# Kernel optimization log

Hardware: AMD Instinct MI355X
Metric: run time of the kernel (lower is better)

## Reference

```python
import jax, jax.numpy as jnp
import numpy as np

H = 4096      # hidden_size (also vocab size of the embedding, per source)
O = 4096      # output_size (also embedding dim, per source)
MAX_LEN = 15


def setup_inputs() -> dict:
    key = jax.random.key(0)
    ks = jax.random.split(key, 16)
    s = 0.02  # init scale
    inp = {
        "input_ids": jax.random.randint(ks[0], (1,), 0, H),
        "hidden": jax.random.normal(ks[1], (1, 1, H), jnp.float32),
        "e_output": jax.random.normal(ks[2], (1, H), jnp.float32),   # unused, kept for signature fidelity
        "e_output_seq": jax.random.normal(ks[3], (MAX_LEN, H), jnp.float32),
        # parameters
        "emb_W": jax.random.normal(ks[4], (H, O), jnp.float32) * s,
        "att_W": jax.random.normal(ks[5], (MAX_LEN, H + O), jnp.float32) * s,
        "att_b": jnp.zeros((MAX_LEN,), jnp.float32),
        "comb_W": jax.random.normal(ks[6], (H, H + O), jnp.float32) * s,
        "comb_b": jnp.zeros((H,), jnp.float32),
        "gru_W_ih": jax.random.normal(ks[7], (3 * H, H), jnp.float32) * s,
        "gru_W_hh": jax.random.normal(ks[8], (3 * H, H), jnp.float32) * s,
        "gru_b_ih": jnp.zeros((3 * H,), jnp.float32),
        "gru_b_hh": jnp.zeros((3 * H,), jnp.float32),
        "out_W": jax.random.normal(ks[9], (O, H), jnp.float32) * s,
        "out_b": jnp.zeros((O,), jnp.float32),
    }
    return inp


def reference(input_ids, hidden, e_output, e_output_seq, emb_W, att_W, att_b,
              comb_W, comb_b, gru_W_ih, gru_W_hh, gru_b_ih, gru_b_hh, out_W, out_b):
    # dropout is identity in eval mode
    emb = emb_W[input_ids[0]][None, :]                       # [1, O]
    h0 = hidden[0]                                            # [1, H]
    att_logits = jnp.concatenate([emb, h0], axis=1) @ att_W.T + att_b
    att_weights = jax.nn.softmax(att_logits, axis=-1)         # [1, MAX_LEN]
    att_applied = att_weights @ e_output_seq                   # [1, H]
    combined = jnp.concatenate([emb, att_applied], axis=1)     # [1, H+O]
    x = jax.nn.relu(combined @ comb_W.T + comb_b)              # [1, H]
    # GRU cell (PyTorch gate order: r, z, n)
    gi = x @ gru_W_ih.T + gru_b_ih                             # [1, 3H]
    gh = h0 @ gru_W_hh.T + gru_b_hh                            # [1, 3H]
    i_r, i_z, i_n = jnp.split(gi, 3, axis=1)
    h_r, h_z, h_n = jnp.split(gh, 3, axis=1)
    r = jax.nn.sigmoid(i_r + h_r)
    z = jax.nn.sigmoid(i_z + h_z)
    n = jnp.tanh(i_n + r * h_n)
    h_new = (1.0 - z) * n + z * h0                             # [1, H]
    out = jax.nn.log_softmax(h_new @ out_W.T + out_b, axis=-1)  # [1, O]
    return out, h_new[None, :, :], att_weights
```

## Files before the change

### kernel.cpp

```cpp
#include <hip/hip_runtime.h>

#define H 4096
#define O 4096
#define HO 8192
#define MAXLEN 15

__device__ __forceinline__ void wave_dot2(const float* __restrict__ w0,
                                          const float* __restrict__ w1,
                                          const float* __restrict__ x,
                                          int n4, int lane,
                                          float& r0, float& r1) {
    const float4* a  = (const float4*)w0;
    const float4* b  = (const float4*)w1;
    const float4* xx = (const float4*)x;
    float acc0 = 0.f, acc1 = 0.f;
    #pragma unroll 4
    for (int i = lane; i < n4; i += 64) {
        float4 xv = xx[i];
        float4 av = a[i];
        float4 bv = b[i];
        acc0 += av.x * xv.x + av.y * xv.y + av.z * xv.z + av.w * xv.w;
        acc1 += bv.x * xv.x + bv.y * xv.y + bv.z * xv.z + bv.w * xv.w;
    }
    #pragma unroll
    for (int off = 32; off; off >>= 1) {
        acc0 += __shfl_down(acc0, off, 64);
        acc1 += __shfl_down(acc1, off, 64);
    }
    r0 = acc0; r1 = acc1;
}

__global__ __launch_bounds__(1024) void k_attlogit(const int* __restrict__ ids,
                                                   const float* __restrict__ hidden,
                                                   const float* __restrict__ embW,
                                                   const float* __restrict__ attW,
                                                   const float* __restrict__ attb,
                                                   float* __restrict__ attlog) {
    __shared__ float sred[16];
    const int tid = threadIdx.x, lane = tid & 63, wave = tid >> 6;
    const int j = blockIdx.x;
    const float* emb = embW + (size_t)ids[0] * O;
    const float4* w4 = (const float4*)(attW + (size_t)j * (H + O));
    const float4* e4 = (const float4*)emb;
    const float4* h4 = (const float4*)hidden;

    float4 wv0 = w4[tid];
    float4 xv0 = e4[tid];
    float4 wv1 = w4[tid + 1024];
    float4 xv1 = h4[tid];
    float acc = wv0.x * xv0.x + wv0.y * xv0.y + wv0.z * xv0.z + wv0.w * xv0.w
              + wv1.x * xv1.x + wv1.y * xv1.y + wv1.z * xv1.z + wv1.w * xv1.w;
    #pragma unroll
    for (int off = 32; off; off >>= 1) acc += __shfl_down(acc, off, 64);
    if (lane == 0) sred[wave] = acc;
    __syncthreads();
    if (tid == 0) {
        float s = 0.f;
        #pragma unroll
        for (int w = 0; w < 16; w++) s += sred[w];
        attlog[j] = s + attb[j];
    }
}

__global__ __launch_bounds__(256) void k_attapply(const int* __restrict__ ids,
                                                  const float* __restrict__ embW,
                                                  const float* __restrict__ attlog,
                                                  const float* __restrict__ eseq,
                                                  float* __restrict__ combined,
                                                  float* __restrict__ out_attw) {
    const int k = blockIdx.x * 256 + threadIdx.x;
    float l[MAXLEN];
    float m = -1e30f;
    #pragma unroll
    for (int j = 0; j < MAXLEN; j++) { l[j] = attlog[j]; m = fmaxf(m, l[j]); }
    float s = 0.f;
    #pragma unroll
    for (int j = 0; j < MAXLEN; j++) { l[j] = __expf(l[j] - m); s += l[j]; }
    const float inv = 1.f / s;

    float acc = 0.f;
    #pragma unroll
    for (int j = 0; j < MAXLEN; j++) acc += l[j] * eseq[j * H + k];
    combined[O + k] = acc * inv;
    combined[k] = embW[(size_t)ids[0] * O + k];
    if (blockIdx.x == 0 && threadIdx.x < MAXLEN) out_attw[threadIdx.x] = l[threadIdx.x] * inv;
}

__global__ __launch_bounds__(512) void k_mv1(const float* __restrict__ combW,
                                             const float* __restrict__ combB,
                                             const float* __restrict__ ghhW,
                                             const float* __restrict__ ghhB,
                                             const float* __restrict__ hidden,
                                             const float* __restrict__ combined,
                                             float* __restrict__ xout,
                                             float* __restrict__ ghout) {
    const int wave = threadIdx.x >> 6, lane = threadIdx.x & 63;
    const int b = blockIdx.x;
    float r0, r1;
    if (b < 256) {
        const int row = b * 16 + wave * 2;
        wave_dot2(combW + (size_t)row * HO, combW + (size_t)(row + 1) * HO,
                  combined, HO >> 2, lane, r0, r1);
        if (lane == 0) {
            xout[row]     = fmaxf(r0 + combB[row], 0.f);
            xout[row + 1] = fmaxf(r1 + combB[row + 1], 0.f);
        }
    } else {
        const int row = (b - 256) * 16 + wave * 2;
        wave_dot2(ghhW + (size_t)row * H, ghhW + (size_t)(row + 1) * H,
                  hidden, H >> 2, lane, r0, r1);
        if (lane == 0) {
            ghout[row]     = r0 + ghhB[row];
            ghout[row + 1] = r1 + ghhB[row + 1];
        }
    }
}

__global__ __launch_bounds__(256) void k_gru(const float* __restrict__ gihW,
                                             const float* __restrict__ gihB,
                                             const float* __restrict__ hidden,
                                             const float* __restrict__ x,
                                             const float* __restrict__ gh,
                                             float* __restrict__ hout,
                                             float* __restrict__ out_h) {
    const int wave = threadIdx.x >> 6, lane = threadIdx.x & 63;
    const int i = blockIdx.x * 4 + wave;
    const float4* w0 = (const float4*)(gihW + (size_t)i * H);
    const float4* w1 = (const float4*)(gihW + (size_t)(i + H) * H);
    const float4* w2 = (const float4*)(gihW + (size_t)(i + 2 * H) * H);
    const float4* x4 = (const float4*)x;
    float a0 = 0.f, a1 = 0.f, a2 = 0.f;
    #pragma unroll 4
    for (int t = lane; t < (H >> 2); t += 64) {
        float4 xv = x4[t];
        float4 v0 = w0[t];
        float4 v1 = w1[t];
        float4 v2 = w2[t];
        a0 += v0.x * xv.x + v0.y * xv.y + v0.z * xv.z + v0.w * xv.w;
        a1 += v1.x * xv.x + v1.y * xv.y + v1.z * xv.z + v1.w * xv.w;
        a2 += v2.x * xv.x + v2.y * xv.y + v2.z * xv.z + v2.w * xv.w;
    }
    #pragma unroll
    for (int off = 32; off; off >>= 1) {
        a0 += __shfl_down(a0, off, 64);
        a1 += __shfl_down(a1, off, 64);
        a2 += __shfl_down(a2, off, 64);
    }
    if (lane == 0) {
        float ir = a0 + gihB[i];
        float iz = a1 + gihB[i + H];
        float in_ = a2 + gihB[i + 2 * H];
        float hr = gh[i], hz = gh[i + H], hn = gh[i + 2 * H];
        float r = 1.f / (1.f + __expf(-(ir + hr)));
        float z = 1.f / (1.f + __expf(-(iz + hz)));
        float n = tanhf(in_ + r * hn);
        float h0 = hidden[i];
        float h = (1.f - z) * n + z * h0;
        hout[i] = h;
        out_h[i] = h;
    }
}

__global__ __launch_bounds__(512) void k_out(const float* __restrict__ outW,
                                             const float* __restrict__ outB,
                                             const float* __restrict__ h,
                                             float* __restrict__ logits) {
    const int wave = threadIdx.x >> 6, lane = threadIdx.x & 63;
    const int row = blockIdx.x * 16 + wave * 2;
    float r0, r1;
    wave_dot2(outW + (size_t)row * H, outW + (size_t)(row + 1) * H, h, H >> 2, lane, r0, r1);
    if (lane == 0) {
        logits[row]     = r0 + outB[row];
        logits[row + 1] = r1 + outB[row + 1];
    }
}

__global__ __launch_bounds__(1024) void k_lsm(const float* __restrict__ logits,
                                              float* __restrict__ out) {
    __shared__ float red[16];
    __shared__ float red2[16];
    const int tid = threadIdx.x, lane = tid & 63, wave = tid >> 6;
    float m = -1e30f;
    for (int k = tid; k < O; k += 1024) m = fmaxf(m, logits[k]);
    #pragma unroll
    for (int off = 32; off; off >>= 1) m = fmaxf(m, __shfl_down(m, off, 64));
    if (lane == 0) red[wave] = m;
    __syncthreads();
    if (tid == 0) {
        float mm = -1e30f;
        for (int j = 0; j < 16; j++) mm = fmaxf(mm, red[j]);
        red[0] = mm;
    }
    __syncthreads();
    m = red[0];
    float s = 0.f;
    for (int k = tid; k < O; k += 1024) s += __expf(logits[k] - m);
    #pragma unroll
    for (int off = 32; off; off >>= 1) s += __shfl_down(s, off, 64);
    if (lane == 0) red2[wave] = s;
    __syncthreads();
    if (tid == 0) {
        float ss = 0.f;
        for (int j = 0; j < 16; j++) ss += red2[j];
        red2[0] = m + logf(ss);
    }
    __syncthreads();
    float lse = red2[0];
    for (int k = tid; k < O; k += 1024) out[k] = logits[k] - lse;
}

extern "C" void kernel_launch(void* const* d_in, const int* in_sizes, int n_in,
                              void* d_out, int out_size, void* d_ws, size_t ws_size,
                              hipStream_t stream) {
    const int*   ids    = (const int*)d_in[0];
    const float* hidden = (const float*)d_in[1];
    const float* eseq   = (const float*)d_in[3];
    const float* embW   = (const float*)d_in[4];
    const float* attW   = (const float*)d_in[5];
    const float* attb   = (const float*)d_in[6];
    const float* combW  = (const float*)d_in[7];
    const float* combB  = (const float*)d_in[8];
    const float* gihW   = (const float*)d_in[9];
    const float* ghhW   = (const float*)d_in[10];
    const float* gihB   = (const float*)d_in[11];
    const float* ghhB   = (const float*)d_in[12];
    const float* outW   = (const float*)d_in[13];
    const float* outB   = (const float*)d_in[14];
    float* out = (float*)d_out;

    float* ws       = (float*)d_ws;
    float* combined = ws;
    float* xbuf     = ws + 8192;
    float* ghbuf    = ws + 12288;
    float* hbuf     = ws + 24576;
    float* logits   = ws + 28672;
    float* attlog   = ws + 32768;

    k_attlogit<<<MAXLEN, 1024, 0, stream>>>(ids, hidden, embW, attW, attb, attlog);
    k_attapply<<<16,     256,  0, stream>>>(ids, embW, attlog, eseq, combined, out + 8192);
    k_mv1     <<<1024,   512,  0, stream>>>(combW, combB, ghhW, ghhB, hidden, combined, xbuf, ghbuf);
    k_gru     <<<1024,   256,  0, stream>>>(gihW, gihB, hidden, xbuf, ghbuf, hbuf, out + 4096);
    k_out     <<<256,    512,  0, stream>>>(outW, outB, hbuf, logits);
    k_lsm     <<<1,      1024, 0, stream>>>(logits, out);
}
```

Measured before the change: 566.0 us.

## Stream GEMV weights through LDS with async double-buffered global_load_lds

```diff
diff --git a/kernel.cpp b/kernel.cpp
--- a/kernel.cpp
+++ b/kernel.cpp
@@ -4,30 +4,53 @@
 #define O 4096
 #define HO 8192
 #define MAXLEN 15
-
-__device__ __forceinline__ void wave_dot2(const float* __restrict__ w0,
-                                          const float* __restrict__ w1,
-                                          const float* __restrict__ x,
-                                          int n4, int lane,
-                                          float& r0, float& r1) {
-    const float4* a  = (const float4*)w0;
-    const float4* b  = (const float4*)w1;
-    const float4* xx = (const float4*)x;
+#define CHUNK 256
+
+typedef const __attribute__((address_space(1))) unsigned int* as1_u32p;
+typedef __attribute__((address_space(3))) unsigned int* as3_u32p;
+
+__device__ __forceinline__ void stage1k(const float* g, float* l) {
+    __builtin_amdgcn_global_load_lds((as1_u32p)g, (as3_u32p)l, 16, 0, 0);
+}
+
+#define WAITV(N) asm volatile("s_waitcnt vmcnt(" #N ")" ::: "memory")
+#define REGION_FENCE() do { asm volatile("" ::: "memory"); __builtin_amdgcn_sched_barrier(0); } while (0)
+
+__device__ __forceinline__ void mv2(const float* __restrict__ W, int row, int K, int NC,
+                                    const float* __restrict__ x, float* sst, int lane,
+                                    float& out0, float& out1) {
+    const float* wr0 = W + (size_t)row * K;
+    const float* wr1 = wr0 + K;
+    stage1k(wr0 + lane * 4, sst);
+    stage1k(wr1 + lane * 4, sst + CHUNK);
+    float4 xcur = *(const float4*)(x + lane * 4);
+    REGION_FENCE();
     float acc0 = 0.f, acc1 = 0.f;
-    #pragma unroll 4
-    for (int i = lane; i < n4; i += 64) {
-        float4 xv = xx[i];
-        float4 av = a[i];
-        float4 bv = b[i];
-        acc0 += av.x * xv.x + av.y * xv.y + av.z * xv.z + av.w * xv.w;
-        acc1 += bv.x * xv.x + bv.y * xv.y + bv.z * xv.z + bv.w * xv.w;
+    for (int t = 0; t < NC; ++t) {
+        float4 xnext = xcur;
+        if (t + 1 < NC) {
+            const int b = ((t + 1) & 1) * (2 * CHUNK);
+            stage1k(wr0 + (size_t)(t + 1) * CHUNK + lane * 4, sst + b);
+            stage1k(wr1 + (size_t)(t + 1) * CHUNK + lane * 4, sst + b + CHUNK);
+            xnext = *(const float4*)(x + (size_t)(t + 1) * CHUNK + lane * 4);
+            WAITV(3);
+        } else {
+            WAITV(0);
+        }
+        __builtin_amdgcn_sched_barrier(0);
+        const int rb = (t & 1) * (2 * CHUNK);
+        float4 a  = *(const float4*)(sst + rb + lane * 4);
+        float4 b4 = *(const float4*)(sst + rb + CHUNK + lane * 4);
+        acc0 += a.x  * xcur.x + a.y  * xcur.y + a.z  * xcur.z + a.w  * xcur.w;
+        acc1 += b4.x * xcur.x + b4.y * xcur.y + b4.z * xcur.z + b4.w * xcur.w;
+        xcur = xnext;
     }
     #pragma unroll
     for (int off = 32; off; off >>= 1) {
         acc0 += __shfl_down(acc0, off, 64);
         acc1 += __shfl_down(acc1, off, 64);
     }
-    r0 = acc0; r1 = acc1;
+    out0 = acc0; out1 = acc1;
 }
 
 __global__ __launch_bounds__(1024) void k_attlogit(const int* __restrict__ ids,
@@ -86,7 +109,7 @@
     if (blockIdx.x == 0 && threadIdx.x < MAXLEN) out_attw[threadIdx.x] = l[threadIdx.x] * inv;
 }
 
-__global__ __launch_bounds__(512) void k_mv1(const float* __restrict__ combW,
+__global__ __launch_bounds__(512) void k_mvA(const float* __restrict__ combW,
                                              const float* __restrict__ combB,
                                              const float* __restrict__ ghhW,
                                              const float* __restrict__ ghhB,
@@ -94,21 +117,20 @@
                                              const float* __restrict__ combined,
                                              float* __restrict__ xout,
                                              float* __restrict__ ghout) {
+    __shared__ __align__(16) float sst[8 * 4 * CHUNK];
     const int wave = threadIdx.x >> 6, lane = threadIdx.x & 63;
-    const int b = blockIdx.x;
+    float* st = sst + wave * 4 * CHUNK;
     float r0, r1;
-    if (b < 256) {
-        const int row = b * 16 + wave * 2;
-        wave_dot2(combW + (size_t)row * HO, combW + (size_t)(row + 1) * HO,
-                  combined, HO >> 2, lane, r0, r1);
+    if (wave < 2) {
+        const int row = blockIdx.x * 4 + wave * 2;
+        mv2(combW, row, HO, HO / CHUNK, combined, st, lane, r0, r1);
         if (lane == 0) {
             xout[row]     = fmaxf(r0 + combB[row], 0.f);
             xout[row + 1] = fmaxf(r1 + combB[row + 1], 0.f);
         }
     } else {
-        const int row = (b - 256) * 16 + wave * 2;
-        wave_dot2(ghhW + (size_t)row * H, ghhW + (size_t)(row + 1) * H,
-                  hidden, H >> 2, lane, r0, r1);
+        const int row = blockIdx.x * 12 + (wave - 2) * 2;
+        mv2(ghhW, row, H, H / CHUNK, hidden, st, lane, r0, r1);
         if (lane == 0) {
             ghout[row]     = r0 + ghhB[row];
             ghout[row + 1] = r1 + ghhB[row + 1];
@@ -116,59 +138,46 @@
     }
 }
 
-__global__ __launch_bounds__(256) void k_gru(const float* __restrict__ gihW,
+__global__ __launch_bounds__(512) void k_mvB(const float* __restrict__ gihW,
                                              const float* __restrict__ gihB,
-                                             const float* __restrict__ hidden,
                                              const float* __restrict__ x,
-                                             const float* __restrict__ gh,
-                                             float* __restrict__ hout,
-                                             float* __restrict__ out_h) {
+                                             float* __restrict__ giout) {
+    __shared__ __align__(16) float sst[8 * 4 * CHUNK];
     const int wave = threadIdx.x >> 6, lane = threadIdx.x & 63;
-    const int i = blockIdx.x * 4 + wave;
-    const float4* w0 = (const float4*)(gihW + (size_t)i * H);
-    const float4* w1 = (const float4*)(gihW + (size_t)(i + H) * H);
-    const float4* w2 = (const float4*)(gihW + (size_t)(i + 2 * H) * H);
-    const float4* x4 = (const float4*)x;
-    float a0 = 0.f, a1 = 0.f, a2 = 0.f;
-    #pragma unroll 4
-    for (int t = lane; t < (H >> 2); t += 64) {
-        float4 xv = x4[t];
-        float4 v0 = w0[t];
-        float4 v1 = w1[t];
-        float4 v2 = w2[t];
-        a0 += v0.x * xv.x + v0.y * xv.y + v0.z * xv.z + v0.w * xv.w;
-        a1 += v1.x * xv.x + v1.y * xv.y + v1.z * xv.z + v1.w * xv.w;
-        a2 += v2.x * xv.x + v2.y * xv.y + v2.z * xv.z + v2.w * xv.w;
-    }
-    #pragma unroll
-    for (int off = 32; off; off >>= 1) {
-        a0 += __shfl_down(a0, off, 64);
-        a1 += __shfl_down(a1, off, 64);
-        a2 += __shfl_down(a2, off, 64);
-    }
+    float* st = sst + wave * 4 * CHUNK;
+    const int row = blockIdx.x * 16 + wave * 2;
+    float r0, r1;
+    mv2(gihW, row, H, H / CHUNK, x, st, lane, r0, r1);
     if (lane == 0) {
-        float ir = a0 + gihB[i];
-        float iz = a1 + gihB[i + H];
-        float in_ = a2 + gihB[i + 2 * H];
-        float hr = gh[i], hz = gh[i + H], hn = gh[i + 2 * H];
-        float r = 1.f / (1.f + __expf(-(ir + hr)));
-        float z = 1.f / (1.f + __expf(-(iz + hz)));
-        float n = tanhf(in_ + r * hn);
-        float h0 = hidden[i];
-        float h = (1.f - z) * n + z * h0;
-        hout[i] = h;
-        out_h[i] = h;
-    }
-}
-
-__global__ __launch_bounds__(512) void k_out(const float* __restrict__ outW,
+        giout[row]     = r0 + gihB[row];
+        giout[row + 1] = r1 + gihB[row + 1];
+    }
+}
+
+__global__ __launch_bounds__(256) void k_gate(const float* __restrict__ gi,
+                                              const float* __restrict__ gh,
+                                              const float* __restrict__ hidden,
+                                              float* __restrict__ hout,
+                                              float* __restrict__ out_h) {
+    const int i = blockIdx.x * 256 + threadIdx.x;
+    float r = 1.f / (1.f + __expf(-(gi[i] + gh[i])));
+    float z = 1.f / (1.f + __expf(-(gi[i + H] + gh[i + H])));
+    float n = tanhf(gi[i + 2 * H] + r * gh[i + 2 * H]);
+    float h = (1.f - z) * n + z * hidden[i];
+    hout[i] = h;
+    out_h[i] = h;
+}
+
+__global__ __launch_bounds__(512) void k_mvC(const float* __restrict__ outW,
                                              const float* __restrict__ outB,
                                              const float* __restrict__ h,
                                              float* __restrict__ logits) {
+    __shared__ __align__(16) float sst[8 * 4 * CHUNK];
     const int wave = threadIdx.x >> 6, lane = threadIdx.x & 63;
+    float* st = sst + wave * 4 * CHUNK;
     const int row = blockIdx.x * 16 + wave * 2;
     float r0, r1;
-    wave_dot2(outW + (size_t)row * H, outW + (size_t)(row + 1) * H, h, H >> 2, lane, r0, r1);
+    mv2(outW, row, H, H / CHUNK, h, st, lane, r0, r1);
     if (lane == 0) {
         logits[row]     = r0 + outB[row];
         logits[row + 1] = r1 + outB[row + 1];
@@ -232,14 +241,16 @@
     float* combined = ws;
     float* xbuf     = ws + 8192;
     float* ghbuf    = ws + 12288;
-    float* hbuf     = ws + 24576;
-    float* logits   = ws + 28672;
-    float* attlog   = ws + 32768;
+    float* gibuf    = ws + 24576;
+    float* hbuf     = ws + 36864;
+    float* logits   = ws + 40960;
+    float* attlog   = ws + 45056;
 
     k_attlogit<<<MAXLEN, 1024, 0, stream>>>(ids, hidden, embW, attW, attb, attlog);
     k_attapply<<<16,     256,  0, stream>>>(ids, embW, attlog, eseq, combined, out + 8192);
-    k_mv1     <<<1024,   512,  0, stream>>>(combW, combB, ghhW, ghhB, hidden, combined, xbuf, ghbuf);
-    k_gru     <<<1024,   256,  0, stream>>>(gihW, gihB, hidden, xbuf, ghbuf, hbuf, out + 4096);
-    k_out     <<<256,    512,  0, stream>>>(outW, outB, hbuf, logits);
+    k_mvA     <<<1024,   512,  0, stream>>>(combW, combB, ghhW, ghhB, hidden, combined, xbuf, ghbuf);
+    k_mvB     <<<768,    512,  0, stream>>>(gihW, gihB, xbuf, gibuf);
+    k_gate    <<<16,     256,  0, stream>>>(gibuf, ghbuf, hidden, hbuf, out + 4096);
+    k_mvC     <<<256,    512,  0, stream>>>(outW, outB, hbuf, logits);
     k_lsm     <<<1,      1024, 0, stream>>>(logits, out);
 }
```

New measurement: 575.5 us. About the same (+1.7%).
